# Optimization experiments

Measured on AMD Instinct MI355X. Metric: run time of the kernel, lower is better.

The kernel has to match this reference:

```python
import jax, jax.numpy as jnp
import numpy as np

WS = 14
NUM_HEADS = 12


def setup_inputs() -> dict:
    key = jax.random.key(0)
    ks = jax.random.split(key, 5)
    B, H, W, C = 16, 56, 56, 768
    x = jax.random.normal(ks[0], (B, H, W, C), dtype=jnp.float32)
    qkv_w = jax.random.normal(ks[1], (3 * C, C), dtype=jnp.float32) * (C ** -0.5)
    qkv_b = jax.random.normal(ks[2], (3 * C,), dtype=jnp.float32) * 0.02
    proj_w = jax.random.normal(ks[3], (C, C), dtype=jnp.float32) * (C ** -0.5)
    proj_b = jax.random.normal(ks[4], (C,), dtype=jnp.float32) * 0.02
    return {"x": x, "qkv_w": qkv_w, "qkv_b": qkv_b, "proj_w": proj_w, "proj_b": proj_b}


def reference(x, qkv_w, qkv_b, proj_w, proj_b):
    B, H, W, C = x.shape
    ws = WS
    h = NUM_HEADS
    hd = C // h
    scale = hd ** -0.5
    N = ws * ws
    # window partition: (B,H,W,C) -> (B*nw, ws*ws, C)
    xw = x.reshape(B, H // ws, ws, W // ws, ws, C)
    xw = xw.transpose(0, 1, 3, 2, 4, 5).reshape(-1, N, C)
    # qkv projection
    qkv = xw @ qkv_w.T + qkv_b                     # (nwB, N, 3C)
    qkv = qkv.reshape(-1, N, 3, h, hd)
    q, k, v = qkv[:, :, 0], qkv[:, :, 1], qkv[:, :, 2]   # (nwB, N, h, hd)
    attn = jnp.einsum('bnhd,bmhd->bhnm', q, k) * scale   # (nwB, h, N, N)
    attn = jax.nn.softmax(attn, axis=-1)
    o = jnp.einsum('bhnm,bmhd->bnhd', attn, v).reshape(-1, N, C)
    o = o @ proj_w.T + proj_b
    # window unpartition: (B*nw, ws, ws, C) -> (B, H, W, C)
    o = o.reshape(B, H // ws, W // ws, ws, ws, C)
    o = o.transpose(0, 1, 3, 2, 4, 5).reshape(B, H, W, C)
    return o
```

## Files before the change

kernel.cpp:

```cpp
#include <hip/hip_runtime.h>

typedef _Float16 half8 __attribute__((ext_vector_type(8)));
typedef _Float16 half4 __attribute__((ext_vector_type(4)));
typedef float f32x4 __attribute__((ext_vector_type(4)));

#define NTOK 196
#define NHEAD 12

__device__ __forceinline__ ushort f2h_u(float f) {
    _Float16 h = (_Float16)f;
    return __builtin_bit_cast(ushort, h);
}

__device__ __forceinline__ void gl_lds16(const ushort* g, ushort* l) {
    __builtin_amdgcn_global_load_lds((const __attribute__((address_space(1))) void*)g,
                                     (__attribute__((address_space(3))) void*)l,
                                     16, 0, 0);
}

__global__ __launch_bounds__(256) void cvt_x(const float* __restrict__ x,
                                             ushort* __restrict__ xb) {
    int idx = blockIdx.x * 256 + threadIdx.x;
    int t   = idx / 192;
    int c   = (idx - t * 192) * 4;
    int win = t / NTOK;
    int n   = t - win * NTOK;
    int b  = win >> 4, wh = (win >> 2) & 3, ww = win & 3;
    int r  = n / 14,  cc = n - r * 14;
    const float4 v = *(const float4*)(x + (((b * 56 + wh * 14 + r) * 56) + ww * 14 + cc) * 768 + c);
    ushort4 o = make_ushort4(f2h_u(v.x), f2h_u(v.y), f2h_u(v.z), f2h_u(v.w));
    *(ushort4*)(xb + t * 768 + c) = o;
}

__global__ __launch_bounds__(256) void cvt_w(const float* __restrict__ qkv_w,
                                             const float* __restrict__ proj_w,
                                             ushort* __restrict__ wq,
                                             ushort* __restrict__ wp) {
    int idx = blockIdx.x * 256 + threadIdx.x;
    int row = idx / 192;
    int c   = (idx - row * 192) * 4;
    const float* src;
    ushort* dst;
    if (row < 2304) { src = qkv_w + row * 768 + c;          dst = wq + row * 768 + c; }
    else            { src = proj_w + (row - 2304) * 768 + c; dst = wp + (row - 2304) * 768 + c; }
    float4 v = *(const float4*)src;
    *(ushort4*)dst = make_ushort4(f2h_u(v.x), f2h_u(v.y), f2h_u(v.z), f2h_u(v.w));
}

__global__ __launch_bounds__(256) void gemm_qkv(const ushort* __restrict__ A,
                                                const ushort* __restrict__ Wq,
                                                const float* __restrict__ qkv_b,
                                                ushort* __restrict__ qbuf,
                                                ushort* __restrict__ kbuf,
                                                ushort* __restrict__ vt,
                                                int MB, int Wc) {
    __shared__ __align__(16) ushort a_s[128 * 32];
    __shared__ __align__(16) ushort b_s[128 * 32];
    const int tid = threadIdx.x, wave = tid >> 6, lane = tid & 63;
    const int quad = lane >> 4, l16 = lane & 15;
    const int mblk = blockIdx.x % MB, nblk = blockIdx.x / MB;
    const int wmo = (wave >> 1) * 64, wno = (wave & 1) * 64;

    f32x4 acc[4][4];
    #pragma unroll
    for (int i = 0; i < 4; ++i)
        #pragma unroll
        for (int j = 0; j < 4; ++j) acc[i][j] = (f32x4){0.f, 0.f, 0.f, 0.f};

    const ushort* Ab = A  + (size_t)mblk * 128 * 768;
    const ushort* Bb = Wq + (size_t)nblk * 128 * 768;

    for (int kt = 0; kt < 24; ++kt) {
        const int k0 = kt * 32;
        #pragma unroll
        for (int p = 0; p < 2; ++p) {
            const int u0 = (p * 4 + wave) * 64;
            const int t  = u0 + lane;
            const int row = t >> 2, c8 = t & 3;
            gl_lds16(Ab + row * 768 + k0 + c8 * 8, a_s + u0 * 8);
            gl_lds16(Bb + row * 768 + k0 + c8 * 8, b_s + u0 * 8);
        }
        __syncthreads();
        half8 bf[4];
        #pragma unroll
        for (int ni = 0; ni < 4; ++ni)
            bf[ni] = *(const half8*)(b_s + (wno + ni * 16 + l16) * 32 + quad * 8);
        #pragma unroll
        for (int mi = 0; mi < 4; ++mi) {
            half8 a = *(const half8*)(a_s + (wmo + mi * 16 + l16) * 32 + quad * 8);
            #pragma unroll
            for (int ni = 0; ni < 4; ++ni)
                acc[mi][ni] = __builtin_amdgcn_mfma_f32_16x16x32_f16(a, bf[ni], acc[mi][ni], 0, 0, 0);
        }
        __syncthreads();
    }

    const int sec = nblk / 6;
    const int cbase = (nblk - sec * 6) * 128 + wno;
    #pragma unroll
    for (int ni = 0; ni < 4; ++ni) {
        const int col_in = cbase + ni * 16 + l16;
        const float bias = qkv_b[sec * 768 + col_in];
        #pragma unroll
        for (int mi = 0; mi < 4; ++mi) {
            #pragma unroll
            for (int r = 0; r < 4; ++r) {
                const int m = mblk * 128 + wmo + mi * 16 + quad * 4 + r;
                const float v = acc[mi][ni][r] + bias;
                if (sec == 0) {
                    qbuf[(size_t)m * 768 + col_in] = f2h_u(v);
                } else if (sec == 1) {
                    kbuf[(size_t)m * 768 + col_in] = f2h_u(v);
                } else {
                    const int win = m / 196, tok = m - win * 196;
                    const int head = col_in >> 6, d = col_in & 63;
                    vt[((size_t)(head * Wc + win) * 64 + d) * 208 + tok] = f2h_u(v);
                }
            }
        }
    }
}

__global__ __launch_bounds__(256) void attn(const ushort* __restrict__ qbuf,
                                            const ushort* __restrict__ kbuf,
                                            const ushort* __restrict__ vt,
                                            ushort* __restrict__ ow, int Wc) {
    __shared__ __align__(16) ushort k_s[2 * 208 * 32];
    __shared__ __align__(16) ushort v_t[64 * 216];
    __shared__ __align__(16) ushort pscr[4 * 512];
    const int tid = threadIdx.x, wave = tid >> 6, lane = tid & 63;
    const int quad = lane >> 4, l16 = lane & 15;
    const int head = blockIdx.x % NHEAD, win = blockIdx.x / NHEAD;

    half8 aq0[4], aq1[4];
    #pragma unroll
    for (int si = 0; si < 4; ++si) {
        int strip = wave + si * 4; if (strip > 12) strip = 12;
        int qtok = strip * 16 + l16; if (qtok > 195) qtok = 195;
        const ushort* qp = qbuf + (size_t)(win * NTOK + qtok) * 768 + head * 64 + quad * 8;
        aq0[si] = *(const half8*)qp;
        aq1[si] = *(const half8*)(qp + 32);
    }

    for (int c = tid; c < 1664; c += 256) {
        const int row = c >> 3, c8 = c & 7;
        half8 val = {};
        if (row < NTOK)
            val = *(const half8*)(kbuf + (size_t)(win * NTOK + row) * 768 + head * 64 + c8 * 8);
        *(half8*)(k_s + ((c8 >> 2) * 208 + row) * 32 + (c8 & 3) * 8) = val;
    }
    {
        const ushort* vsrc = vt + (size_t)(head * Wc + win) * 64 * 208;
        for (int c = tid; c < 1664; c += 256) {
            const int d = c / 26, c8 = c - d * 26;
            *(half8*)(v_t + d * 216 + c8 * 8) = *(const half8*)(vsrc + d * 208 + c8 * 8);
        }
    }
    __syncthreads();

    ushort* ps = pscr + wave * 512;
    for (int si = 0; si < 4; ++si) {
        const int strip = wave + si * 4;
        if (strip > 12) break;
        f32x4 sacc[13];
        #pragma unroll
        for (int nt = 0; nt < 13; ++nt) sacc[nt] = (f32x4){0.f, 0.f, 0.f, 0.f};
        #pragma unroll
        for (int nt = 0; nt < 13; ++nt) {
            const int krow = (nt * 16 + l16) * 32 + quad * 8;
            half8 kb0 = *(const half8*)(k_s + krow);
            half8 kb1 = *(const half8*)(k_s + 208 * 32 + krow);
            sacc[nt] = __builtin_amdgcn_mfma_f32_16x16x32_f16(aq0[si], kb0, sacc[nt], 0, 0, 0);
            sacc[nt] = __builtin_amdgcn_mfma_f32_16x16x32_f16(aq1[si], kb1, sacc[nt], 0, 0, 0);
        }
        float P[13][4], linv[4];
        #pragma unroll
        for (int r = 0; r < 4; ++r) {
            float sv[13];
            float mx = -1e30f;
            #pragma unroll
            for (int nt = 0; nt < 13; ++nt) {
                float s = sacc[nt][r] * 0.125f;
                if (nt == 12 && l16 >= 4) s = -1e30f;
                sv[nt] = s;
                mx = fmaxf(mx, s);
            }
            mx = fmaxf(mx, __shfl_xor(mx, 1));
            mx = fmaxf(mx, __shfl_xor(mx, 2));
            mx = fmaxf(mx, __shfl_xor(mx, 4));
            mx = fmaxf(mx, __shfl_xor(mx, 8));
            float l = 0.f;
            #pragma unroll
            for (int nt = 0; nt < 13; ++nt) {
                float e = __expf(sv[nt] - mx);
                P[nt][r] = e;
                l += e;
            }
            l += __shfl_xor(l, 1);
            l += __shfl_xor(l, 2);
            l += __shfl_xor(l, 4);
            l += __shfl_xor(l, 8);
            linv[r] = 1.f / l;
        }
        f32x4 oacc[4];
        #pragma unroll
        for (int dt = 0; dt < 4; ++dt) oacc[dt] = (f32x4){0.f, 0.f, 0.f, 0.f};
        #pragma unroll
        for (int ks = 0; ks < 6; ++ks) {
            #pragma unroll
            for (int h = 0; h < 2; ++h) {
                const int nt = ks * 2 + h;
                #pragma unroll
                for (int r = 0; r < 4; ++r)
                    ps[(quad * 4 + r) * 32 + h * 16 + l16] = f2h_u(P[nt][r]);
            }
            half8 a = *(const half8*)(ps + l16 * 32 + quad * 8);
            #pragma unroll
            for (int dt = 0; dt < 4; ++dt) {
                half8 vb = *(const half8*)(v_t + (dt * 16 + l16) * 216 + ks * 32 + quad * 8);
                oacc[dt] = __builtin_amdgcn_mfma_f32_16x16x32_f16(a, vb, oacc[dt], 0, 0, 0);
            }
        }
        {
            #pragma unroll
            for (int r = 0; r < 4; ++r)
                ps[(quad * 4 + r) * 32 + l16] = f2h_u(P[12][r]);
            half4 a4 = *(const half4*)(ps + l16 * 32 + quad * 4);
            #pragma unroll
            for (int dt = 0; dt < 4; ++dt) {
                half4 vb4 = *(const half4*)(v_t + (dt * 16 + l16) * 216 + 192 + quad * 4);
                oacc[dt] = __builtin_amdgcn_mfma_f32_16x16x16f16(a4, vb4, oacc[dt], 0, 0, 0);
            }
        }
        const int sb = strip * 16;
        #pragma unroll
        for (int r = 0; r < 4; ++r) {
            const int token = sb + quad * 4 + r;
            if (token < NTOK) {
                #pragma unroll
                for (int dt = 0; dt < 4; ++dt)
                    ow[(size_t)(win * NTOK + token) * 768 + head * 64 + dt * 16 + l16] =
                        f2h_u(oacc[dt][r] * linv[r]);
            }
        }
    }
}

__global__ __launch_bounds__(256) void proj_k(const ushort* __restrict__ ow,
                                              const ushort* __restrict__ wp,
                                              const float* __restrict__ pb,
                                              float* __restrict__ out) {
    __shared__ __align__(16) ushort a_s[128 * 32];
    __shared__ __align__(16) ushort b_s[128 * 32];
    const int tid = threadIdx.x, wave = tid >> 6, lane = tid & 63;
    const int quad = lane >> 4, l16 = lane & 15;
    const int mblk = blockIdx.x / 6, nblk = blockIdx.x - mblk * 6;
    const int wmo = (wave >> 1) * 64, wno = (wave & 1) * 64;

    f32x4 acc[4][4];
    #pragma unroll
    for (int i = 0; i < 4; ++i)
        #pragma unroll
        for (int j = 0; j < 4; ++j) acc[i][j] = (f32x4){0.f, 0.f, 0.f, 0.f};

    for (int kt = 0; kt < 24; ++kt) {
        const int k0 = kt * 32;
        #pragma unroll
        for (int p = 0; p < 2; ++p) {
            const int u0 = (p * 4 + wave) * 64;
            const int t  = u0 + lane;
            const int row = t >> 2, c8 = t & 3;
            gl_lds16(ow + (size_t)(mblk * 128 + row) * 768 + k0 + c8 * 8, a_s + u0 * 8);
            gl_lds16(wp + (size_t)(nblk * 128 + row) * 768 + k0 + c8 * 8, b_s + u0 * 8);
        }
        __syncthreads();
        half8 bf[4];
        #pragma unroll
        for (int ni = 0; ni < 4; ++ni)
            bf[ni] = *(const half8*)(b_s + (wno + ni * 16 + l16) * 32 + quad * 8);
        #pragma unroll
        for (int mi = 0; mi < 4; ++mi) {
            half8 a = *(const half8*)(a_s + (wmo + mi * 16 + l16) * 32 + quad * 8);
            #pragma unroll
            for (int ni = 0; ni < 4; ++ni)
                acc[mi][ni] = __builtin_amdgcn_mfma_f32_16x16x32_f16(a, bf[ni], acc[mi][ni], 0, 0, 0);
        }
        __syncthreads();
    }
    #pragma unroll
    for (int mi = 0; mi < 4; ++mi) {
        #pragma unroll
        for (int r = 0; r < 4; ++r) {
            int grow = mblk * 128 + wmo + mi * 16 + quad * 4 + r;
            int wnd = grow / 196, tok = grow - wnd * 196;
            int b = wnd >> 4, wh = (wnd >> 2) & 3, ww = wnd & 3;
            int rr = tok / 14, cc = tok - rr * 14;
            float* orow = out + ((b * 56 + wh * 14 + rr) * 56 + ww * 14 + cc) * 768;
            #pragma unroll
            for (int ni = 0; ni < 4; ++ni) {
                int col = nblk * 128 + wno + ni * 16 + l16;
                orow[col] = acc[mi][ni][r] + pb[col];
            }
        }
    }
}

extern "C" void kernel_launch(void* const* d_in, const int* in_sizes, int n_in,
                              void* d_out, int out_size, void* d_ws, size_t ws_size,
                              hipStream_t stream) {
    const float* x      = (const float*)d_in[0];
    const float* qkv_w  = (const float*)d_in[1];
    const float* qkv_b  = (const float*)d_in[2];
    const float* proj_w = (const float*)d_in[3];
    const float* proj_b = (const float*)d_in[4];
    float* out = (float*)d_out;

    char* ws = (char*)d_ws;
    ushort* xb = (ushort*)ws;
    ushort* wq = (ushort*)(ws + 77070336);
    ushort* wp = (ushort*)(ws + 80609280);
    char* dyn = ws + 81788928;

    size_t avail = ws_size > 81788928u ? ws_size - 81788928u : 0;
    int Wc = 256;
    while (Wc > 32 && (size_t)Wc * 921600u > avail) Wc >>= 1;
    const int nchunk = 256 / Wc;
    const int MB = Wc * NTOK / 128;

    ushort* qbuf = (ushort*)dyn;
    ushort* kbuf = qbuf + (size_t)Wc * NTOK * 768;
    ushort* vt   = kbuf + (size_t)Wc * NTOK * 768;

    cvt_x<<<37632, 256, 0, stream>>>(x, xb);
    cvt_w<<<2304, 256, 0, stream>>>(qkv_w, proj_w, wq, wp);
    hipMemsetAsync(vt, 0, (size_t)Wc * NHEAD * 64 * 208 * 2, stream);

    for (int c = 0; c < nchunk; ++c) {
        const ushort* xbc = xb + (size_t)c * Wc * NTOK * 768;
        ushort* owc = xb + (size_t)c * Wc * NTOK * 768;
        gemm_qkv<<<MB * 18, 256, 0, stream>>>(xbc, wq, qkv_b, qbuf, kbuf, vt, MB, Wc);
        attn<<<Wc * NHEAD, 256, 0, stream>>>(qbuf, kbuf, vt, owc, Wc);
    }
    proj_k<<<392 * 6, 256, 0, stream>>>(xb, wp, proj_b, out);
}
```

Before: 910.9 us.

## Use 256x256 tiles with double-buffered swizzled LDS pipeline for QKV and proj GEMMs

Replaces the 128x128, 4-wave GEMM tiles of both the QKV and projection kernels with a shared 256x256-tile, 8-wave main loop that uses K-steps of 64. The loop double-buffers LDS, swizzles LDS addresses with XOR to avoid bank conflicts, and interleaves global-to-LDS staging with four MFMA phases under explicit barriers and setprio. The aim is more data reuse per LDS byte and hiding global load latency behind compute. In exchange it uses 128KB of LDS and many accumulator registers per block, so only one block fits per CU, and the minimum chunk size rises to 64 windows.

```diff
diff --git a/kernel.cpp b/kernel.cpp
--- a/kernel.cpp
+++ b/kernel.cpp
@@ -47,66 +47,147 @@
     *(ushort4*)dst = make_ushort4(f2h_u(v.x), f2h_u(v.y), f2h_u(v.z), f2h_u(v.w));
 }
 
-__global__ __launch_bounds__(256) void gemm_qkv(const ushort* __restrict__ A,
-                                                const ushort* __restrict__ Wq,
-                                                const float* __restrict__ qkv_b,
-                                                ushort* __restrict__ qbuf,
-                                                ushort* __restrict__ kbuf,
-                                                ushort* __restrict__ vt,
-                                                int MB, int Wc) {
-    __shared__ __align__(16) ushort a_s[128 * 32];
-    __shared__ __align__(16) ushort b_s[128 * 32];
+__device__ __forceinline__ void kloop256(const ushort* __restrict__ Ab,
+                                         const ushort* __restrict__ Bb,
+                                         ushort* sh,
+                                         f32x4 (&acc)[8][4]) {
     const int tid = threadIdx.x, wave = tid >> 6, lane = tid & 63;
     const int quad = lane >> 4, l16 = lane & 15;
+    const int wm = wave >> 2, wn = wave & 3;
+    const int sr = lane >> 3;
+    const int sc = ((lane & 7) ^ sr) * 8;
+    const int rd_xor = (l16 & 7) << 4;
+    const int rowB0 = (wn & 1) * 64;
+    half8 Ar[4][2], Br[2][2][2];
+
+#define STAGE_Q(srcK, ldsHalf, q) \
+    gl_lds16((srcK) + ((q) * 64 + wave * 8 + sr) * 768 + sc, \
+             (ldsHalf) + (((q) & 1) * 64 + wave * 8) * 64)
+
+#define LD_A(QM, aB) \
+    _Pragma("unroll") for (int mi = 0; mi < 4; ++mi) \
+    _Pragma("unroll") for (int kk = 0; kk < 2; ++kk) \
+        Ar[mi][kk] = *(const half8*)((aB) + \
+            (((((QM) * 64 + mi * 16 + l16) * 128) + kk * 64 + quad * 16) ^ rd_xor))
+
+#define LD_B(QN, bB) \
+    _Pragma("unroll") for (int nj = 0; nj < 2; ++nj) \
+    _Pragma("unroll") for (int kk = 0; kk < 2; ++kk) \
+        Br[QN][nj][kk] = *(const half8*)((bB) + \
+            ((((rowB0 + (QN) * 32 + nj * 16 + l16) * 128) + kk * 64 + quad * 16) ^ rd_xor))
+
+#define MFMA_Q(QM, QN) \
+    _Pragma("unroll") for (int mi = 0; mi < 4; ++mi) \
+    _Pragma("unroll") for (int nj = 0; nj < 2; ++nj) \
+    _Pragma("unroll") for (int kk = 0; kk < 2; ++kk) \
+        acc[(QM) * 4 + mi][(QN) * 2 + nj] = __builtin_amdgcn_mfma_f32_16x16x32_f16( \
+            Ar[mi][kk], Br[QN][nj][kk], acc[(QM) * 4 + mi][(QN) * 2 + nj], 0, 0, 0)
+
+#define PH_SYNC_PRE() do { \
+    __builtin_amdgcn_s_barrier(); \
+    asm volatile("s_waitcnt lgkmcnt(0)" ::: "memory"); \
+    __builtin_amdgcn_sched_barrier(0); \
+    __builtin_amdgcn_s_setprio(1); } while (0)
+
+#define PH_SYNC_POST() do { \
+    __builtin_amdgcn_s_setprio(0); \
+    __builtin_amdgcn_sched_barrier(0); \
+    __builtin_amdgcn_s_barrier(); } while (0)
+
+    {
+        ushort* a0 = sh;
+        ushort* b0 = sh + 32768;
+        #pragma unroll
+        for (int q = 0; q < 4; ++q) STAGE_Q(Ab, a0 + (q >> 1) * 8192, q);
+        #pragma unroll
+        for (int q = 0; q < 4; ++q) STAGE_Q(Bb, b0 + (q >> 1) * 8192, q);
+        ushort* a1 = sh + 16384;
+        ushort* b1 = sh + 32768 + 16384;
+        STAGE_Q(Ab + 64, a1, 0);
+        STAGE_Q(Ab + 64, a1 + 8192, 2);
+        #pragma unroll
+        for (int q = 0; q < 4; ++q) STAGE_Q(Bb + 64, b1 + (q >> 1) * 8192, q);
+        asm volatile("s_waitcnt vmcnt(6)" ::: "memory");
+        __builtin_amdgcn_s_barrier();
+    }
+
+    const int NT = 12;
+    for (int T = 0; T < NT; ++T) {
+        const int buf = T & 1;
+        const char* aB = (const char*)(sh + buf * 16384 + wm * 8192);
+        const char* bB = (const char*)(sh + 32768 + buf * 16384 + (wn >> 1) * 8192);
+        ushort* aN = sh + (buf ^ 1) * 16384;
+        ushort* aC = sh + buf * 16384;
+        ushort* bC = sh + 32768 + buf * 16384;
+        const bool p1 = (T + 1 < NT), p2 = (T + 2 < NT);
+
+        LD_A(0, aB); LD_B(0, bB);
+        if (p1) { STAGE_Q(Ab + (T + 1) * 64, aN, 1);
+                  STAGE_Q(Ab + (T + 1) * 64, aN + 8192, 3); }
+        PH_SYNC_PRE(); MFMA_Q(0, 0); PH_SYNC_POST();
+
+        LD_B(1, bB);
+        if (p2) { STAGE_Q(Ab + (T + 2) * 64, aC, 0);
+                  STAGE_Q(Ab + (T + 2) * 64, aC + 8192, 2); }
+        PH_SYNC_PRE(); MFMA_Q(0, 1); PH_SYNC_POST();
+
+        LD_A(1, aB);
+        if (p2) { STAGE_Q(Bb + (T + 2) * 64, bC, 0);
+                  STAGE_Q(Bb + (T + 2) * 64, bC, 1); }
+        PH_SYNC_PRE(); MFMA_Q(1, 1); PH_SYNC_POST();
+
+        if (p2) { STAGE_Q(Bb + (T + 2) * 64, bC + 8192, 2);
+                  STAGE_Q(Bb + (T + 2) * 64, bC + 8192, 3); }
+        if (p2)      { asm volatile("s_waitcnt vmcnt(6)" ::: "memory"); }
+        else if (p1) { asm volatile("s_waitcnt vmcnt(0)" ::: "memory"); }
+        __builtin_amdgcn_s_barrier();
+        __builtin_amdgcn_s_setprio(1);
+        MFMA_Q(1, 0);
+        __builtin_amdgcn_s_setprio(0);
+        __builtin_amdgcn_sched_barrier(0);
+        __builtin_amdgcn_s_barrier();
+    }
+#undef STAGE_Q
+#undef LD_A
+#undef LD_B
+#undef MFMA_Q
+#undef PH_SYNC_PRE
+#undef PH_SYNC_POST
+}
+
+__global__ __launch_bounds__(512, 1) void gemm_qkv(const ushort* __restrict__ A,
+                                                   const ushort* __restrict__ Wq,
+                                                   const float* __restrict__ qkv_b,
+                                                   ushort* __restrict__ qbuf,
+                                                   ushort* __restrict__ kbuf,
+                                                   ushort* __restrict__ vt,
+                                                   int MB, int Wc) {
+    __shared__ __align__(16) ushort sh[65536];
+    const int tid = threadIdx.x, wave = tid >> 6, lane = tid & 63;
+    const int quad = lane >> 4, l16 = lane & 15;
+    const int wm = wave >> 2, wn = wave & 3;
     const int mblk = blockIdx.x % MB, nblk = blockIdx.x / MB;
-    const int wmo = (wave >> 1) * 64, wno = (wave & 1) * 64;
-
-    f32x4 acc[4][4];
+
+    f32x4 acc[8][4];
     #pragma unroll
-    for (int i = 0; i < 4; ++i)
+    for (int i = 0; i < 8; ++i)
         #pragma unroll
         for (int j = 0; j < 4; ++j) acc[i][j] = (f32x4){0.f, 0.f, 0.f, 0.f};
 
-    const ushort* Ab = A  + (size_t)mblk * 128 * 768;
-    const ushort* Bb = Wq + (size_t)nblk * 128 * 768;
-
-    for (int kt = 0; kt < 24; ++kt) {
-        const int k0 = kt * 32;
-        #pragma unroll
-        for (int p = 0; p < 2; ++p) {
-            const int u0 = (p * 4 + wave) * 64;
-            const int t  = u0 + lane;
-            const int row = t >> 2, c8 = t & 3;
-            gl_lds16(Ab + row * 768 + k0 + c8 * 8, a_s + u0 * 8);
-            gl_lds16(Bb + row * 768 + k0 + c8 * 8, b_s + u0 * 8);
-        }
-        __syncthreads();
-        half8 bf[4];
-        #pragma unroll
-        for (int ni = 0; ni < 4; ++ni)
-            bf[ni] = *(const half8*)(b_s + (wno + ni * 16 + l16) * 32 + quad * 8);
-        #pragma unroll
-        for (int mi = 0; mi < 4; ++mi) {
-            half8 a = *(const half8*)(a_s + (wmo + mi * 16 + l16) * 32 + quad * 8);
-            #pragma unroll
-            for (int ni = 0; ni < 4; ++ni)
-                acc[mi][ni] = __builtin_amdgcn_mfma_f32_16x16x32_f16(a, bf[ni], acc[mi][ni], 0, 0, 0);
-        }
-        __syncthreads();
-    }
-
-    const int sec = nblk / 6;
-    const int cbase = (nblk - sec * 6) * 128 + wno;
+    kloop256(A + (size_t)mblk * 256 * 768, Wq + (size_t)nblk * 256 * 768, sh, acc);
+
+    const int sec = nblk / 3;
+    const int colq = nblk - sec * 3;
     #pragma unroll
-    for (int ni = 0; ni < 4; ++ni) {
-        const int col_in = cbase + ni * 16 + l16;
+    for (int nj = 0; nj < 4; ++nj) {
+        const int col_in = colq * 256 + wn * 64 + nj * 16 + l16;
         const float bias = qkv_b[sec * 768 + col_in];
         #pragma unroll
-        for (int mi = 0; mi < 4; ++mi) {
+        for (int mi = 0; mi < 8; ++mi) {
             #pragma unroll
             for (int r = 0; r < 4; ++r) {
-                const int m = mblk * 128 + wmo + mi * 16 + quad * 4 + r;
-                const float v = acc[mi][ni][r] + bias;
+                const int m = mblk * 256 + wm * 128 + mi * 16 + quad * 4 + r;
+                const float v = acc[mi][nj][r] + bias;
                 if (sec == 0) {
                     qbuf[(size_t)m * 768 + col_in] = f2h_u(v);
                 } else if (sec == 1) {
@@ -246,60 +327,37 @@
     }
 }
 
-__global__ __launch_bounds__(256) void proj_k(const ushort* __restrict__ ow,
-                                              const ushort* __restrict__ wp,
-                                              const float* __restrict__ pb,
-                                              float* __restrict__ out) {
-    __shared__ __align__(16) ushort a_s[128 * 32];
-    __shared__ __align__(16) ushort b_s[128 * 32];
+__global__ __launch_bounds__(512, 1) void proj_k(const ushort* __restrict__ ow,
+                                                 const ushort* __restrict__ wp,
+                                                 const float* __restrict__ pb,
+                                                 float* __restrict__ out) {
+    __shared__ __align__(16) ushort sh[65536];
     const int tid = threadIdx.x, wave = tid >> 6, lane = tid & 63;
     const int quad = lane >> 4, l16 = lane & 15;
-    const int mblk = blockIdx.x / 6, nblk = blockIdx.x - mblk * 6;
-    const int wmo = (wave >> 1) * 64, wno = (wave & 1) * 64;
-
-    f32x4 acc[4][4];
+    const int wm = wave >> 2, wn = wave & 3;
+    const int mblk = blockIdx.x % 196, nblk = blockIdx.x / 196;
+
+    f32x4 acc[8][4];
     #pragma unroll
-    for (int i = 0; i < 4; ++i)
+    for (int i = 0; i < 8; ++i)
         #pragma unroll
         for (int j = 0; j < 4; ++j) acc[i][j] = (f32x4){0.f, 0.f, 0.f, 0.f};
 
-    for (int kt = 0; kt < 24; ++kt) {
-        const int k0 = kt * 32;
-        #pragma unroll
-        for (int p = 0; p < 2; ++p) {
-            const int u0 = (p * 4 + wave) * 64;
-            const int t  = u0 + lane;
-            const int row = t >> 2, c8 = t & 3;
-            gl_lds16(ow + (size_t)(mblk * 128 + row) * 768 + k0 + c8 * 8, a_s + u0 * 8);
-            gl_lds16(wp + (size_t)(nblk * 128 + row) * 768 + k0 + c8 * 8, b_s + u0 * 8);
-        }
-        __syncthreads();
-        half8 bf[4];
-        #pragma unroll
-        for (int ni = 0; ni < 4; ++ni)
-            bf[ni] = *(const half8*)(b_s + (wno + ni * 16 + l16) * 32 + quad * 8);
-        #pragma unroll
-        for (int mi = 0; mi < 4; ++mi) {
-            half8 a = *(const half8*)(a_s + (wmo + mi * 16 + l16) * 32 + quad * 8);
-            #pragma unroll
-            for (int ni = 0; ni < 4; ++ni)
-                acc[mi][ni] = __builtin_amdgcn_mfma_f32_16x16x32_f16(a, bf[ni], acc[mi][ni], 0, 0, 0);
-        }
-        __syncthreads();
-    }
+    kloop256(ow + (size_t)mblk * 256 * 768, wp + (size_t)nblk * 256 * 768, sh, acc);
+
     #pragma unroll
-    for (int mi = 0; mi < 4; ++mi) {
+    for (int mi = 0; mi < 8; ++mi) {
         #pragma unroll
         for (int r = 0; r < 4; ++r) {
-            int grow = mblk * 128 + wmo + mi * 16 + quad * 4 + r;
+            int grow = mblk * 256 + wm * 128 + mi * 16 + quad * 4 + r;
             int wnd = grow / 196, tok = grow - wnd * 196;
             int b = wnd >> 4, wh = (wnd >> 2) & 3, ww = wnd & 3;
             int rr = tok / 14, cc = tok - rr * 14;
             float* orow = out + ((b * 56 + wh * 14 + rr) * 56 + ww * 14 + cc) * 768;
             #pragma unroll
-            for (int ni = 0; ni < 4; ++ni) {
-                int col = nblk * 128 + wno + ni * 16 + l16;
-                orow[col] = acc[mi][ni][r] + pb[col];
+            for (int nj = 0; nj < 4; ++nj) {
+                int col = nblk * 256 + wn * 64 + nj * 16 + l16;
+                orow[col] = acc[mi][nj][r] + pb[col];
             }
         }
     }
@@ -323,9 +381,9 @@
 
     size_t avail = ws_size > 81788928u ? ws_size - 81788928u : 0;
     int Wc = 256;
-    while (Wc > 32 && (size_t)Wc * 921600u > avail) Wc >>= 1;
+    while (Wc > 64 && (size_t)Wc * 921600u > avail) Wc >>= 1;
     const int nchunk = 256 / Wc;
-    const int MB = Wc * NTOK / 128;
+    const int MB = Wc * NTOK / 256;
 
     ushort* qbuf = (ushort*)dyn;
     ushort* kbuf = qbuf + (size_t)Wc * NTOK * 768;
@@ -338,8 +396,8 @@
     for (int c = 0; c < nchunk; ++c) {
         const ushort* xbc = xb + (size_t)c * Wc * NTOK * 768;
         ushort* owc = xb + (size_t)c * Wc * NTOK * 768;
-        gemm_qkv<<<MB * 18, 256, 0, stream>>>(xbc, wq, qkv_b, qbuf, kbuf, vt, MB, Wc);
+        gemm_qkv<<<MB * 9, 512, 0, stream>>>(xbc, wq, qkv_b, qbuf, kbuf, vt, MB, Wc);
         attn<<<Wc * NHEAD, 256, 0, stream>>>(qbuf, kbuf, vt, owc, Wc);
     }
-    proj_k<<<392 * 6, 256, 0, stream>>>(xb, wp, proj_b, out);
-}
+    proj_k<<<196 * 3, 512, 0, stream>>>(xb, wp, proj_b, out);
+}
```

Result: faster. 890.9 us (-2.2%).
